# Kernel optimization log

Hardware: AMD Instinct MI355X
Metric: run time of the kernel (lower is better)

## Reference

```python
import jax, jax.numpy as jnp
import numpy as np

# ProbSparseAttention (Informer-style), mask_flag=False, factor=10, scale=None,
# output_attention=False, dropout never applied in forward.
# L = 2048 -> U_part = u = 10 * ceil(log(2048)) = 80.
U_TOP = 80


def setup_inputs() -> dict:
    key = jax.random.key(0)
    kq, kk, kv, ki = jax.random.split(key, 4)
    B, L, H, D = 2, 2048, 8, 64
    sample_k = U_TOP
    queries = jax.random.normal(kq, (B, L, H, D), dtype=jnp.float32)
    keys = jax.random.normal(kk, (B, L, H, D), dtype=jnp.float32)
    values = jax.random.normal(kv, (B, L, H, D), dtype=jnp.float32)
    # replaces torch.randint(low=0, high=min(L_Q, L_K), size=(L_Q, sample_k))
    index_sample = jax.random.randint(ki, (L, sample_k), 0, L, dtype=jnp.int32)
    return {"queries": queries, "keys": keys, "values": values,
            "index_sample": index_sample}


def reference(queries, keys, values, index_sample):
    B, L_Q, H, D = queries.shape
    L_K = keys.shape[1]
    u = U_TOP  # n_top queries kept (== sample_k here)

    # [B, L, H, D] -> [B, H, L, D]
    Q = jnp.transpose(queries, (0, 2, 1, 3))
    K = jnp.transpose(keys, (0, 2, 1, 3))
    V = jnpp_transpose = jnp.transpose(values, (0, 2, 1, 3))

    # --- _prob_QK: gather sampled keys per query position ---
    # K_sample[b,h,l,s,:] = K[b,h,index_sample[l,s],:]  -> [B,H,L_Q,sample_k,D]
    K_sample = K[:, :, index_sample, :]
    # Q_K_sample: [B,H,L_Q,sample_k]
    Q_K_sample = jnp.einsum('bhld,bhlsd->bhls', Q, K_sample)
    # sparsity measure M = max - mean(sum/L_K)
    M = Q_K_sample.max(axis=-1) - Q_K_sample.sum(axis=-1) / L_K  # [B,H,L_Q]
    _, M_top = jax.lax.top_k(M, u)  # [B,H,u] indices of top queries

    # Q_reduce: [B,H,u,D]
    Q_reduce = jnp.take_along_axis(Q, M_top[..., None], axis=2)
    # sparse scores against ALL keys: [B,H,u,L_K]
    scale = 1.0 / np.sqrt(D).astype(np.float32)
    scores = jnp.einsum('bhud,bhkd->bhuk', Q_reduce, K) * scale

    # --- initial context (mask_flag=False): mean of V broadcast over u slots ---
    V_mean = V.mean(axis=2)  # [B,H,D]
    context = jnp.broadcast_to(V_mean[:, :, None, :], (B, H, u, D))

    # --- update context at selected slots ---
    attn = jax.nn.softmax(scores, axis=-1)          # [B,H,u,L_K]
    upd = jnp.einsum('bhuk,bhkd->bhud', attn, V)    # [B,H,u,D]
    # original clamps index into [0, L_slot-1] where L_slot = u
    idx = jnp.clip(M_top, 0, u - 1)
    b_idx = jnp.arange(B)[:, None, None]
    h_idx = jnp.arange(H)[None, :, None]
    context = context.at[b_idx, h_idx, idx, :].set(upd)

    # [B,H,u,D] -> [B,u,H,D]
    return jnp.transpose(context, (0, 2, 1, 3))
```

## Files before the change

kernel.cpp:

```cpp
#include <hip/hip_runtime.h>
#include <math.h>

#define LQ 2048
#define NH 8
#define DD 64
#define SK 80
#define UTOP 80
#define NB 2
#define CH 32
#define CK2 64
#define CKS 32

__global__ __launch_bounds__(256) void kA_M(const float* __restrict__ Q,
                                            const float* __restrict__ K,
                                            const float* __restrict__ V,
                                            const int* __restrict__ idxs,
                                            float* __restrict__ M,
                                            float* __restrict__ out) {
    __shared__ float4 red[16][16];
    int tid = threadIdx.x;
    int x = blockIdx.x;
    if (x < 16) {
        int b = x >> 3, h = x & 7;
        int d4 = tid & 15, ls = tid >> 4;
        const float4* V4 = (const float4*)V;
        float4 s = make_float4(0.f, 0.f, 0.f, 0.f);
        for (int i = 0; i < 128; ++i) {
            int l = (i << 4) + ls;
            float4 v = V4[(((size_t)(b * LQ + l) * NH + h) << 4) + d4];
            s.x += v.x; s.y += v.y; s.z += v.z; s.w += v.w;
        }
        red[ls][d4] = s;
        __syncthreads();
        if (ls == 0) {
            float4 t = red[0][d4];
            for (int k = 1; k < 16; ++k) {
                float4 r = red[k][d4];
                t.x += r.x; t.y += r.y; t.z += r.z; t.w += r.w;
            }
            t.x *= (1.f / 2048.f); t.y *= (1.f / 2048.f);
            t.z *= (1.f / 2048.f); t.w *= (1.f / 2048.f);
            red[0][d4] = t;
        }
        __syncthreads();
        float4* out4 = (float4*)out;
        for (int f = tid; f < UTOP * 16; f += 256) {
            int r = f >> 4, dd = f & 15;
            out4[(((size_t)(b * UTOP + r) * NH + h) << 4) + dd] = red[0][dd];
        }
        return;
    }
    x -= 16;
    int h = x & 7;
    int b = (x >> 3) & 1;
    int l = ((x >> 4) << 2) + (tid >> 6);
    int lane = tid & 63;
    int g = lane >> 4;
    int t = lane & 15;
    const float4* Q4 = (const float4*)Q;
    const float4* K4 = (const float4*)K;
    float4 q4 = Q4[(((size_t)(b * LQ + l) * NH + h) << 4) + t];
    const int* idxrow = idxs + l * SK;
    int kidx[20];
#pragma unroll
    for (int it = 0; it < 20; ++it) kidx[it] = idxrow[(it << 2) + g];
    __builtin_amdgcn_sched_barrier(0);
    float4 kb[20];
#pragma unroll
    for (int it = 0; it < 20; ++it)
        kb[it] = K4[(((size_t)(b * LQ + kidx[it]) * NH + h) << 4) + t];
    __builtin_amdgcn_sched_barrier(0);
    float maxv = -INFINITY, sumv = 0.f;
#pragma unroll
    for (int it = 0; it < 20; ++it) {
        float4 k4 = kb[it];
        float p = q4.x * k4.x + q4.y * k4.y + q4.z * k4.z + q4.w * k4.w;
        p += __int_as_float(__builtin_amdgcn_update_dpp(
                 0, __float_as_int(p), 177, 0xf, 0xf, false));
        p += __int_as_float(__builtin_amdgcn_update_dpp(
                 0, __float_as_int(p), 78, 0xf, 0xf, false));
        p += __int_as_float(__builtin_amdgcn_update_dpp(
                 0, __float_as_int(p), 0x141, 0xf, 0xf, false));
        p += __int_as_float(__builtin_amdgcn_update_dpp(
                 0, __float_as_int(p), 0x140, 0xf, 0xf, false));
        maxv = fmaxf(maxv, p);
        sumv += p;
    }
    maxv = fmaxf(maxv, __shfl_xor(maxv, 16));
    maxv = fmaxf(maxv, __shfl_xor(maxv, 32));
    sumv += __shfl_xor(sumv, 16);
    sumv += __shfl_xor(sumv, 32);
    if (lane == 0) M[(b * NH + h) * LQ + l] = maxv - sumv * (1.f / 2048.f);
}

__global__ __launch_bounds__(256) void kB_topk(const float* __restrict__ M,
                                               int* __restrict__ Mtop,
                                               int* __restrict__ Winfo) {
    int bh = blockIdx.x;
    int tid = threadIdx.x;
    int lane = tid & 63, w = tid >> 6;
    __shared__ unsigned long long keys[LQ];
    __shared__ int hist[256];
    __shared__ int wavered[4];
    __shared__ int s_need;
    __shared__ unsigned long long s_prefix;
    __shared__ int s_cnt;
    __shared__ unsigned long long s_win;
    const float* Mrow = M + bh * LQ;
#pragma unroll
    for (int i = 0; i < 8; ++i) {
        int e = i * 256 + tid;
        unsigned int bits = __float_as_uint(Mrow[e]);
        bits ^= (unsigned int)(((int)bits >> 31)) | 0x80000000u;
        keys[e] = ((unsigned long long)bits << 16) | (unsigned int)(2047 - e);
    }
    if (tid == 0) { s_need = UTOP; s_prefix = 0ull; s_cnt = 0; s_win = ~0ull; }
    __syncthreads();
#pragma unroll
    for (int pass = 0; pass < 6; ++pass) {
        int shift = 40 - pass * 8;
        int need = s_need;
        unsigned long long pref = s_prefix;
        hist[tid] = 0;
        __syncthreads();
        unsigned long long prefmask = ~((1ull << (shift + 8)) - 1ull);
#pragma unroll
        for (int i = 0; i < 8; ++i) {
            unsigned long long k = keys[i * 256 + tid];
            if ((k & prefmask) == pref)
                atomicAdd(&hist[(int)((k >> shift) & 255)], 1);
        }
        __syncthreads();
        int b = 255 - tid;
        int v = hist[b];
        int x = v;
#pragma unroll
        for (int off = 1; off < 64; off <<= 1) {
            int y = __shfl_up(x, off);
            if (lane >= off) x += y;
        }
        if (lane == 63) wavered[w] = x;
        __syncthreads();
        int add = 0;
        for (int ww = 0; ww < w; ++ww) add += wavered[ww];
        int C = x + add;
        if (C >= need && C - v < need) {
            s_need = need - (C - v);
            s_prefix = pref | ((unsigned long long)b << shift);
        }
        __syncthreads();
    }
    unsigned long long kth = s_prefix;
#pragma unroll
    for (int i = 0; i < 8; ++i) {
        unsigned long long k = keys[i * 256 + tid];
        if (k >= kth) {
            int slot = atomicAdd(&s_cnt, 1);
            int q = 2047 - (int)(k & 0xffffu);
            Mtop[bh * UTOP + slot] = q;
            if (q >= UTOP - 1) atomicMin(&s_win, k);
        }
    }
    __syncthreads();
    if (tid == 0) Winfo[bh] = 2047 - (int)(s_win & 0xffffu);
}

__global__ __launch_bounds__(256) void kD_attn(const float* __restrict__ Q,
                                               const float* __restrict__ K,
                                               const float* __restrict__ V,
                                               const int* __restrict__ Mtop,
                                               float* __restrict__ part_m,
                                               float* __restrict__ part_l,
                                               float* __restrict__ part_acc) {
    int code = blockIdx.x & 15;
    int b = code & 1, h = code >> 1;
    int bhl = b * NH + h;
    int c = blockIdx.x >> 4;
    __shared__ int topl[UTOP];
    __shared__ __align__(16) float Qs[UTOP][68];
    __shared__ __align__(16) float Ks[CKS][68];
    __shared__ __align__(16) float Vs[CKS][68];
    __shared__ __align__(16) float Ps[UTOP][36];
    int tid = threadIdx.x;
    if (tid < UTOP) topl[tid] = Mtop[bhl * UTOP + tid];
    __syncthreads();
    for (int f = tid; f < UTOP * 16; f += 256) {
        int u = f >> 4, t4 = f & 15;
        const float4* src = (const float4*)(Q + (((size_t)(b * LQ + topl[u]) * NH + h) << 6));
        *((float4*)&Qs[u][t4 << 2]) = src[t4];
    }
    int i = tid >> 4, j = tid & 15;
    const float scale = 0.125f;
    float4 acc[5];
    float m_run[5], l_run[5];
#pragma unroll
    for (int n = 0; n < 5; ++n) {
        acc[n] = make_float4(0.f, 0.f, 0.f, 0.f);
        m_run[n] = -INFINITY;
        l_run[n] = 0.f;
    }
    for (int sc = 0; sc < 2; ++sc) {
        __syncthreads();
        int kbase = c * CK2 + sc * CKS;
        for (int f = tid; f < CKS * 16; f += 256) {
            int k = f >> 4, t4 = f & 15;
            const float4* srck = (const float4*)(K + (((size_t)(b * LQ + kbase + k) * NH + h) << 6));
            *((float4*)&Ks[k][t4 << 2]) = srck[t4];
            const float4* srcv = (const float4*)(V + (((size_t)(b * LQ + kbase + k) * NH + h) << 6));
            *((float4*)&Vs[k][t4 << 2]) = srcv[t4];
        }
        __syncthreads();
        float s0[5], s1[5];
#pragma unroll
        for (int n = 0; n < 5; ++n) { s0[n] = 0.f; s1[n] = 0.f; }
#pragma unroll
        for (int d4 = 0; d4 < 16; ++d4) {
            float4 ka = *((float4*)&Ks[j][d4 << 2]);
            float4 kb = *((float4*)&Ks[j + 16][d4 << 2]);
#pragma unroll
            for (int n = 0; n < 5; ++n) {
                float4 q4 = *((float4*)&Qs[i * 5 + n][d4 << 2]);
                s0[n] += q4.x * ka.x + q4.y * ka.y + q4.z * ka.z + q4.w * ka.w;
                s1[n] += q4.x * kb.x + q4.y * kb.y + q4.z * kb.z + q4.w * kb.w;
            }
        }
        float m32[5], l32[5];
#pragma unroll
        for (int n = 0; n < 5; ++n) {
            float a = s0[n] * scale, bb = s1[n] * scale;
            float m = fmaxf(a, bb);
#pragma unroll
            for (int off = 1; off < 16; off <<= 1) m = fmaxf(m, __shfl_xor(m, off, 16));
            float p0 = __expf(a - m), p1 = __expf(bb - m);
            float ls = p0 + p1;
#pragma unroll
            for (int off = 1; off < 16; off <<= 1) ls += __shfl_xor(ls, off, 16);
            int u = i * 5 + n;
            Ps[u][j] = p0;
            Ps[u][j + 16] = p1;
            m32[n] = m;
            l32[n] = ls;
        }
        __syncthreads();
        float4 pv[5];
#pragma unroll
        for (int n = 0; n < 5; ++n) pv[n] = make_float4(0.f, 0.f, 0.f, 0.f);
#pragma unroll
        for (int kt = 0; kt < 4; ++kt) {
            float4 pA[5], pB[5];
#pragma unroll
            for (int n = 0; n < 5; ++n) {
                pA[n] = *((float4*)&Ps[i * 5 + n][kt * 8]);
                pB[n] = *((float4*)&Ps[i * 5 + n][kt * 8 + 4]);
            }
#pragma unroll
            for (int kk = 0; kk < 8; ++kk) {
                float4 v4 = *((float4*)&Vs[kt * 8 + kk][j << 2]);
#pragma unroll
                for (int n = 0; n < 5; ++n) {
                    float p = (kk < 4) ? ((float*)&pA[n])[kk] : ((float*)&pB[n])[kk - 4];
                    pv[n].x += p * v4.x; pv[n].y += p * v4.y;
                    pv[n].z += p * v4.z; pv[n].w += p * v4.w;
                }
            }
        }
#pragma unroll
        for (int n = 0; n < 5; ++n) {
            float m_new = fmaxf(m_run[n], m32[n]);
            float fo = __expf(m_run[n] - m_new);
            float fn = __expf(m32[n] - m_new);
            l_run[n] = l_run[n] * fo + l32[n] * fn;
            acc[n].x = acc[n].x * fo + fn * pv[n].x;
            acc[n].y = acc[n].y * fo + fn * pv[n].y;
            acc[n].z = acc[n].z * fo + fn * pv[n].z;
            acc[n].w = acc[n].w * fo + fn * pv[n].w;
            m_run[n] = m_new;
        }
    }
#pragma unroll
    for (int n = 0; n < 5; ++n) {
        int u = i * 5 + n;
        size_t base = ((size_t)(bhl * CH + c) * UTOP + u);
        if (j == 0) {
            part_m[base] = m_run[n];
            part_l[base] = l_run[n];
        }
        *((float4*)&part_acc[base * DD + (j << 2)]) = acc[n];
    }
}

__global__ __launch_bounds__(64) void kE_combine(const float* __restrict__ part_m,
                                                 const float* __restrict__ part_l,
                                                 const float* __restrict__ part_acc,
                                                 const int* __restrict__ Mtop,
                                                 const int* __restrict__ Winfo,
                                                 float* __restrict__ out) {
    int bhl = blockIdx.x & 15;
    int u = blockIdx.x >> 4;
    int q = Mtop[bhl * UTOP + u];
    int r;
    if (q < UTOP - 1) r = q;
    else { if (q != Winfo[bhl]) return; r = UTOP - 1; }
    int lane = threadIdx.x;
    float mc = -INFINITY, lc = 0.f;
    if (lane < CH) {
        mc = part_m[(size_t)(bhl * CH + lane) * UTOP + u];
        lc = part_l[(size_t)(bhl * CH + lane) * UTOP + u];
    }
    float m = mc;
#pragma unroll
    for (int off = 1; off < 64; off <<= 1) m = fmaxf(m, __shfl_xor(m, off));
    float alpha = __expf(mc - m);
    float lsum = lc * alpha;
#pragma unroll
    for (int off = 1; off < 64; off <<= 1) lsum += __shfl_xor(lsum, off);
    float accd = 0.f;
    for (int c = 0; c < CH; ++c) {
        float a = __shfl(alpha, c);
        accd += a * part_acc[((size_t)(bhl * CH + c) * UTOP + u) * DD + lane];
    }
    int b = bhl >> 3, h = bhl & 7;
    out[(((size_t)(b * UTOP + r)) * NH + h) * DD + lane] = accd / lsum;
}

extern "C" void kernel_launch(void* const* d_in, const int* in_sizes, int n_in,
                              void* d_out, int out_size, void* d_ws, size_t ws_size,
                              hipStream_t stream) {
    const float* Q = (const float*)d_in[0];
    const float* K = (const float*)d_in[1];
    const float* V = (const float*)d_in[2];
    const int* idxs = (const int*)d_in[3];
    float* out = (float*)d_out;

    char* base = (char*)d_ws;
    float* M        = (float*)(base + 0);
    int*   Mtop     = (int*)  (base + 131072);
    int*   Winfo    = (int*)  (base + 136192);
    float* part_m   = (float*)(base + 136256);
    float* part_l   = (float*)(base + 300096);
    float* part_acc = (float*)(base + 463936);

    kA_M   <<<8192 + 16, 256, 0, stream>>>(Q, K, V, idxs, M, out);
    kB_topk<<<16,   256, 0, stream>>>(M, Mtop, Winfo);
    kD_attn<<<16 * CH, 256, 0, stream>>>(Q, K, V, Mtop, part_m, part_l, part_acc);
    kE_combine<<<16 * UTOP, 64, 0, stream>>>(part_m, part_l, part_acc, Mtop, Winfo, out);
}
```

Measured before the change: 133.4 us.

## Remap sampled-QK kernel so each block covers all heads of one query row

The M-computation kernel now gives each block one (batch, query) position across all 8 heads, so the 16 heads × 16 lanes read a full contiguous 2 KB K row per sampled index instead of a single head's 256 B slice. Each thread handles 40 samples in 4 chunks of 10 loads rather than 20 at once, which lowers register pressure. Max and sum are combined across the two sample slots through shared memory and a block barrier. The grid shrinks from 8192 to 4096 compute blocks, each with more work per thread and one added sync.

```diff
diff --git a/kernel.cpp b/kernel.cpp
--- a/kernel.cpp
+++ b/kernel.cpp
@@ -18,6 +18,7 @@
                                             float* __restrict__ M,
                                             float* __restrict__ out) {
     __shared__ float4 red[16][16];
+    __shared__ float smax[2][NH], ssum[2][NH];
     int tid = threadIdx.x;
     int x = blockIdx.x;
     if (x < 16) {
@@ -51,46 +52,50 @@
         return;
     }
     x -= 16;
-    int h = x & 7;
-    int b = (x >> 3) & 1;
-    int l = ((x >> 4) << 2) + (tid >> 6);
-    int lane = tid & 63;
-    int g = lane >> 4;
-    int t = lane & 15;
+    int b = x & 1;
+    int l = x >> 1;
+    int slot = tid >> 7;
+    int hq = (tid >> 4) & 7;
+    int t = tid & 15;
     const float4* Q4 = (const float4*)Q;
     const float4* K4 = (const float4*)K;
-    float4 q4 = Q4[(((size_t)(b * LQ + l) * NH + h) << 4) + t];
+    float4 q4 = Q4[(((size_t)(b * LQ + l) * NH + hq) << 4) + t];
     const int* idxrow = idxs + l * SK;
-    int kidx[20];
-#pragma unroll
-    for (int it = 0; it < 20; ++it) kidx[it] = idxrow[(it << 2) + g];
-    __builtin_amdgcn_sched_barrier(0);
-    float4 kb[20];
-#pragma unroll
-    for (int it = 0; it < 20; ++it)
-        kb[it] = K4[(((size_t)(b * LQ + kidx[it]) * NH + h) << 4) + t];
+    int sid[40];
+#pragma unroll
+    for (int i = 0; i < 40; ++i) sid[i] = idxrow[(i << 1) + slot];
     __builtin_amdgcn_sched_barrier(0);
     float maxv = -INFINITY, sumv = 0.f;
 #pragma unroll
-    for (int it = 0; it < 20; ++it) {
-        float4 k4 = kb[it];
-        float p = q4.x * k4.x + q4.y * k4.y + q4.z * k4.z + q4.w * k4.w;
-        p += __int_as_float(__builtin_amdgcn_update_dpp(
-                 0, __float_as_int(p), 177, 0xf, 0xf, false));
-        p += __int_as_float(__builtin_amdgcn_update_dpp(
-                 0, __float_as_int(p), 78, 0xf, 0xf, false));
-        p += __int_as_float(__builtin_amdgcn_update_dpp(
-                 0, __float_as_int(p), 0x141, 0xf, 0xf, false));
-        p += __int_as_float(__builtin_amdgcn_update_dpp(
-                 0, __float_as_int(p), 0x140, 0xf, 0xf, false));
-        maxv = fmaxf(maxv, p);
-        sumv += p;
-    }
-    maxv = fmaxf(maxv, __shfl_xor(maxv, 16));
-    maxv = fmaxf(maxv, __shfl_xor(maxv, 32));
-    sumv += __shfl_xor(sumv, 16);
-    sumv += __shfl_xor(sumv, 32);
-    if (lane == 0) M[(b * NH + h) * LQ + l] = maxv - sumv * (1.f / 2048.f);
+    for (int ch = 0; ch < 4; ++ch) {
+        float4 kb[10];
+#pragma unroll
+        for (int i = 0; i < 10; ++i)
+            kb[i] = K4[(((size_t)(b * LQ + sid[ch * 10 + i]) * NH + hq) << 4) + t];
+        __builtin_amdgcn_sched_barrier(0);
+#pragma unroll
+        for (int i = 0; i < 10; ++i) {
+            float4 k4 = kb[i];
+            float p = q4.x * k4.x + q4.y * k4.y + q4.z * k4.z + q4.w * k4.w;
+            p += __int_as_float(__builtin_amdgcn_update_dpp(
+                     0, __float_as_int(p), 177, 0xf, 0xf, false));
+            p += __int_as_float(__builtin_amdgcn_update_dpp(
+                     0, __float_as_int(p), 78, 0xf, 0xf, false));
+            p += __int_as_float(__builtin_amdgcn_update_dpp(
+                     0, __float_as_int(p), 0x141, 0xf, 0xf, false));
+            p += __int_as_float(__builtin_amdgcn_update_dpp(
+                     0, __float_as_int(p), 0x140, 0xf, 0xf, false));
+            maxv = fmaxf(maxv, p);
+            sumv += p;
+        }
+    }
+    if (t == 0) { smax[slot][hq] = maxv; ssum[slot][hq] = sumv; }
+    __syncthreads();
+    if (tid < NH) {
+        float mv = fmaxf(smax[0][tid], smax[1][tid]);
+        float sv = ssum[0][tid] + ssum[1][tid];
+        M[(b * NH + tid) * LQ + l] = mv - sv * (1.f / 2048.f);
+    }
 }
 
 __global__ __launch_bounds__(256) void kB_topk(const float* __restrict__ M,
@@ -340,7 +345,7 @@
     float* part_l   = (float*)(base + 300096);
     float* part_acc = (float*)(base + 463936);
 
-    kA_M   <<<8192 + 16, 256, 0, stream>>>(Q, K, V, idxs, M, out);
+    kA_M   <<<16 + NB * LQ, 256, 0, stream>>>(Q, K, V, idxs, M, out);
     kB_topk<<<16,   256, 0, stream>>>(M, Mtop, Winfo);
     kD_attn<<<16 * CH, 256, 0, stream>>>(Q, K, V, Mtop, part_m, part_l, part_acc);
     kE_combine<<<16 * UTOP, 64, 0, stream>>>(part_m, part_l, part_acc, Mtop, Winfo, out);
```

After: 139.6 us. 1.05x slower.

## Fuse split-K combine into attention kernel via last-block atomic counter

Applied to the files above, without the earlier changes.

Removes the separate combine kernel launch. Each attention block now bumps a per-(b,h) atomic counter after writing its partial softmax state, and the last block to finish merges all CH partials and writes the output. The counters are reset in the first kernel. This saves one launch and its gap, but the final merge for each head runs serially in a single block, which may lengthen the tail.

```diff
diff --git a/kernel.cpp b/kernel.cpp
--- a/kernel.cpp
+++ b/kernel.cpp
@@ -16,11 +16,13 @@
                                             const float* __restrict__ V,
                                             const int* __restrict__ idxs,
                                             float* __restrict__ M,
-                                            float* __restrict__ out) {
+                                            float* __restrict__ out,
+                                            int* __restrict__ cnt) {
     __shared__ float4 red[16][16];
     int tid = threadIdx.x;
     int x = blockIdx.x;
     if (x < 16) {
+        if (tid == 0) cnt[x] = 0;
         int b = x >> 3, h = x & 7;
         int d4 = tid & 15, ls = tid >> 4;
         const float4* V4 = (const float4*)V;
@@ -169,9 +171,12 @@
                                                const float* __restrict__ K,
                                                const float* __restrict__ V,
                                                const int* __restrict__ Mtop,
+                                               const int* __restrict__ Winfo,
                                                float* __restrict__ part_m,
                                                float* __restrict__ part_l,
-                                               float* __restrict__ part_acc) {
+                                               float* __restrict__ part_acc,
+                                               int* __restrict__ cnt,
+                                               float* __restrict__ out) {
     int code = blockIdx.x & 15;
     int b = code & 1, h = code >> 1;
     int bhl = b * NH + h;
@@ -181,6 +186,7 @@
     __shared__ __align__(16) float Ks[CKS][68];
     __shared__ __align__(16) float Vs[CKS][68];
     __shared__ __align__(16) float Ps[UTOP][36];
+    __shared__ int s_last;
     int tid = threadIdx.x;
     if (tid < UTOP) topl[tid] = Mtop[bhl * UTOP + tid];
     __syncthreads();
@@ -287,40 +293,43 @@
         }
         *((float4*)&part_acc[base * DD + (j << 2)]) = acc[n];
     }
-}
-
-__global__ __launch_bounds__(64) void kE_combine(const float* __restrict__ part_m,
-                                                 const float* __restrict__ part_l,
-                                                 const float* __restrict__ part_acc,
-                                                 const int* __restrict__ Mtop,
-                                                 const int* __restrict__ Winfo,
-                                                 float* __restrict__ out) {
-    int bhl = blockIdx.x & 15;
-    int u = blockIdx.x >> 4;
-    int q = Mtop[bhl * UTOP + u];
-    int r;
-    if (q < UTOP - 1) r = q;
-    else { if (q != Winfo[bhl]) return; r = UTOP - 1; }
-    int lane = threadIdx.x;
-    float mc = -INFINITY, lc = 0.f;
-    if (lane < CH) {
-        mc = part_m[(size_t)(bhl * CH + lane) * UTOP + u];
-        lc = part_l[(size_t)(bhl * CH + lane) * UTOP + u];
-    }
-    float m = mc;
-#pragma unroll
-    for (int off = 1; off < 64; off <<= 1) m = fmaxf(m, __shfl_xor(m, off));
-    float alpha = __expf(mc - m);
-    float lsum = lc * alpha;
-#pragma unroll
-    for (int off = 1; off < 64; off <<= 1) lsum += __shfl_xor(lsum, off);
-    float accd = 0.f;
-    for (int c = 0; c < CH; ++c) {
-        float a = __shfl(alpha, c);
-        accd += a * part_acc[((size_t)(bhl * CH + c) * UTOP + u) * DD + lane];
-    }
-    int b = bhl >> 3, h = bhl & 7;
-    out[(((size_t)(b * UTOP + r)) * NH + h) * DD + lane] = accd / lsum;
+    __threadfence();
+    __syncthreads();
+    if (tid == 0) {
+        int old = atomicAdd(&cnt[bhl], 1);
+        s_last = (old == CH - 1) ? 1 : 0;
+    }
+    __syncthreads();
+    if (!s_last) return;
+    __threadfence();
+    if (tid < UTOP) {
+        int u = tid;
+        float mu = -INFINITY;
+        for (int c2 = 0; c2 < CH; ++c2)
+            mu = fmaxf(mu, part_m[((size_t)(bhl * CH + c2)) * UTOP + u]);
+        float ls = 0.f;
+        for (int c2 = 0; c2 < CH; ++c2) {
+            float a = __expf(part_m[((size_t)(bhl * CH + c2)) * UTOP + u] - mu);
+            ls += part_l[((size_t)(bhl * CH + c2)) * UTOP + u] * a;
+            Qs[u][c2] = a;
+        }
+        Ps[u][0] = ls;
+    }
+    __syncthreads();
+    int wq = Winfo[bhl];
+    for (int w2 = tid; w2 < UTOP * DD; w2 += 256) {
+        int u = w2 >> 6, d = w2 & 63;
+        int qq = topl[u];
+        int r;
+        if (qq < UTOP - 1) r = qq;
+        else { if (qq != wq) continue; r = UTOP - 1; }
+        float acc2 = 0.f;
+#pragma unroll 8
+        for (int c2 = 0; c2 < CH; ++c2)
+            acc2 += Qs[u][c2] *
+                    part_acc[(((size_t)(bhl * CH + c2)) * UTOP + u) * DD + d];
+        out[(((size_t)(b * UTOP + r)) * NH + h) * DD + d] = acc2 / Ps[u][0];
+    }
 }
 
 extern "C" void kernel_launch(void* const* d_in, const int* in_sizes, int n_in,
@@ -339,9 +348,10 @@
     float* part_m   = (float*)(base + 136256);
     float* part_l   = (float*)(base + 300096);
     float* part_acc = (float*)(base + 463936);
-
-    kA_M   <<<8192 + 16, 256, 0, stream>>>(Q, K, V, idxs, M, out);
+    int*   cnt      = (int*)  (base + 10949696);
+
+    kA_M   <<<8192 + 16, 256, 0, stream>>>(Q, K, V, idxs, M, out, cnt);
     kB_topk<<<16,   256, 0, stream>>>(M, Mtop, Winfo);
-    kD_attn<<<16 * CH, 256, 0, stream>>>(Q, K, V, Mtop, part_m, part_l, part_acc);
-    kE_combine<<<16 * UTOP, 64, 0, stream>>>(part_m, part_l, part_acc, Mtop, Winfo, out);
+    kD_attn<<<16 * CH, 256, 0, stream>>>(Q, K, V, Mtop, Winfo,
+                                         part_m, part_l, part_acc, cnt, out);
 }
```

After: 195.0 us. 1.46x slower.
